# Optimization experiments

Measured on AMD Instinct MI355X. Metric: run time of the kernel, lower is better.

The kernel has to match this reference:

```python
import jax, jax.numpy as jnp
import numpy as np

HEAD_DIM = 64
N_HEADS = 16


def _rope_tables(seq_len, head_dim):
    pos = np.arange(seq_len, dtype=np.float32)
    freq = np.arange(0, head_dim, 2, dtype=np.float32) / head_dim
    inv_freq = 1.0 / (10000.0 ** freq)
    angles = np.outer(pos, inv_freq)                     # [S, D/2]
    angles = np.repeat(angles, 2, axis=-1)               # [S, D] interleaved
    return jnp.asarray(np.cos(angles)), jnp.asarray(np.sin(angles))


def _rotate_half(x):
    x1 = x[..., ::2]
    x2 = x[..., 1::2]
    return jnp.stack((-x2, x1), axis=-1).reshape(x.shape)


def _apply_rope(x, cos, sin):
    # x: [B, H, S, D]; cos/sin: [S, D]
    return x * cos + _rotate_half(x) * sin


def setup_inputs() -> dict:
    key = jax.random.key(0)
    ks = jax.random.split(key, 5)
    d = N_HEADS * HEAD_DIM
    B, S = 4, 2048
    s = 1.0 / np.sqrt(d)
    return {
        "x": jax.random.normal(ks[0], (B, S, d), dtype=jnp.float32),
        "Wq": jax.random.normal(ks[1], (d, d), dtype=jnp.float32) * s,
        "bq": jnp.zeros((d,), jnp.float32),
        "Wk": jax.random.normal(ks[2], (d, d), dtype=jnp.float32) * s,
        "bk": jnp.zeros((d,), jnp.float32),
        "Wv": jax.random.normal(ks[3], (d, d), dtype=jnp.float32) * s,
        "bv": jnp.zeros((d,), jnp.float32),
        "Wo": jax.random.normal(ks[4], (d, d), dtype=jnp.float32) * s,
        "bo": jnp.zeros((d,), jnp.float32),
    }


def reference(x, Wq, bq, Wk, bk, Wv, bv, Wo, bo):
    B, S, d = x.shape
    H, D = N_HEADS, HEAD_DIM
    scale = D ** -0.5

    q = (x @ Wq + bq).reshape(B, S, H, D).transpose(0, 2, 1, 3)  # [B,H,S,D]
    k = (x @ Wk + bk).reshape(B, S, H, D).transpose(0, 2, 1, 3)
    v = (x @ Wv + bv).reshape(B, S, H, D).transpose(0, 2, 1, 3)

    cos, sin = _rope_tables(S, D)
    q = _apply_rope(q, cos, sin)
    k = _apply_rope(k, cos, sin)

    att = jnp.einsum("bhqd,bhkd->bhqk", q, k) * scale            # [B,H,S,S]
    causal = jnp.tril(jnp.ones((S, S), dtype=bool))
    att = jnp.where(causal, att, -jnp.inf)
    att = jax.nn.softmax(att, axis=-1)

    y = jnp.einsum("bhqk,bhkd->bhqd", att, v)                    # [B,H,S,D]
    y = y.transpose(0, 2, 1, 3).reshape(B, S, d)
    return y @ Wo + bo
```

## Files before the change

### kernel.cpp

```cpp
#include <hip/hip_runtime.h>

typedef __bf16 bf16;
typedef __bf16 bf16x2 __attribute__((ext_vector_type(2)));
typedef __bf16 bf16x4 __attribute__((ext_vector_type(4)));
typedef __bf16 bf16x8 __attribute__((ext_vector_type(8)));
typedef float  f32x4  __attribute__((ext_vector_type(4)));

#define MFMA16(a,b,c) __builtin_amdgcn_mfma_f32_16x16x32_bf16(a,b,c,0,0,0)
#define GLL16(g, l) __builtin_amdgcn_global_load_lds( \
    (const __attribute__((address_space(1))) unsigned char*)(g), \
    (__attribute__((address_space(3))) unsigned char*)(l), 16, 0, 0)
#define BARRIER() asm volatile("s_barrier" ::: "memory")
#define DRAIN(n)  asm volatile("s_waitcnt vmcnt(" #n ")" ::: "memory")

constexpr int SEQ   = 2048;
constexpr int NH    = 16;
constexpr int HD    = 64;
constexpr int BATCH = 4;
constexpr int DM    = 1024;
constexpr size_t TEN = (size_t)BATCH * NH * SEQ * HD;

__global__ __launch_bounds__(256) void k_prep(const float* __restrict__ x,
                                              const float* __restrict__ W0,
                                              const float* __restrict__ W1,
                                              const float* __restrict__ W2,
                                              const float* __restrict__ W3,
                                              bf16* __restrict__ Wt_all,
                                              bf16* __restrict__ xb) {
    __shared__ float T[64][65];
    const int z = blockIdx.z;
    const int t = threadIdx.x;
    if (z == 4) {
        const int bi = blockIdx.y * 16 + blockIdx.x;
#pragma unroll
        for (int c = 0; c < 16; c++) {
            const size_t idx = (size_t)c * 524288 + ((size_t)bi * 256 + t) * 8;
            float4 f0 = *(const float4*)(x + idx);
            float4 f1 = *(const float4*)(x + idx + 4);
            bf16x8 o;
            o[0] = (bf16)f0.x; o[1] = (bf16)f0.y; o[2] = (bf16)f0.z; o[3] = (bf16)f0.w;
            o[4] = (bf16)f1.x; o[5] = (bf16)f1.y; o[6] = (bf16)f1.z; o[7] = (bf16)f1.w;
            *(bf16x8*)(xb + idx) = o;
        }
        return;
    }
    const float* W = (z == 0) ? W0 : (z == 1) ? W1 : (z == 2) ? W2 : W3;
    bf16* Wt = Wt_all + (size_t)z * DM * DM;
    const int kb = blockIdx.x, nb = blockIdx.y;
    const int rl = t >> 2, seg = t & 3;
    const float* src = W + (size_t)(kb * 64 + rl) * DM + nb * 64 + seg * 16;
#pragma unroll
    for (int j4 = 0; j4 < 4; j4++) {
        float4 f = *(const float4*)(src + j4 * 4);
        T[rl][seg * 16 + j4 * 4 + 0] = f.x;
        T[rl][seg * 16 + j4 * 4 + 1] = f.y;
        T[rl][seg * 16 + j4 * 4 + 2] = f.z;
        T[rl][seg * 16 + j4 * 4 + 3] = f.w;
    }
    __syncthreads();
    bf16* dst = Wt + (size_t)(nb * 64 + rl) * DM + kb * 64 + seg * 16;
    bf16x8 o0, o1;
#pragma unroll
    for (int j = 0; j < 8; j++) {
        o0[j] = (bf16)T[seg * 16 + j][rl];
        o1[j] = (bf16)T[seg * 16 + 8 + j][rl];
    }
    *(bf16x8*)dst = o0;
    *(bf16x8*)(dst + 8) = o1;
}

template <int MODE>
__global__ __launch_bounds__(512, 1) void k_gemm(const bf16* __restrict__ A,
                                                 const bf16* __restrict__ Wt0,
                                                 const float* __restrict__ b0,
                                                 const float* __restrict__ b1,
                                                 const float* __restrict__ b2,
                                                 bf16* __restrict__ vt,
                                                 void* __restrict__ out) {
    __shared__ __align__(1024) bf16 LA[3][16384];
    __shared__ __align__(1024) bf16 LB[2][8192];
    const int t = threadIdx.x;
    const int w = t >> 6, lane = t & 63, quad = lane >> 4, l16 = lane & 15;
    const int bm = blockIdx.x * 256;
    const int by = blockIdx.y;
    const int z  = (MODE == 0) ? (by >> 3) : 0;
    const int bn = (MODE == 0) ? ((by & 7) * 128) : (by * 128);
    const bf16* Wt = Wt0 + (size_t)z * DM * DM;
    const float* bias = (z == 0) ? b0 : (z == 1) ? b1 : b2;
    const int wm = (w >> 2) * 128, wn = (w & 3) * 32;

    const int srow = lane >> 3;
    const int sseg = (lane & 7) ^ srow;
    const bf16* gA = A  + (size_t)(bm + w * 8 + srow) * DM + sseg * 8;
    const bf16* gB = Wt + (size_t)(bn + w * 8 + srow) * DM + sseg * 8;

#define STGA_P(lp, tt, c) do { \
    const bf16* _g = gA + (size_t)(c) * 128 * DM + (size_t)(tt) * 64; \
    bf16* _l = (lp) + ((c) * 16 + w) * 512; \
    GLL16(_g, _l); GLL16(_g + 64 * DM, _l + 4096); \
} while (0)
#define STGB_P(lp, tt) do { \
    const bf16* _g = gB + (size_t)(tt) * 64; \
    bf16* _l = (lp) + w * 512; \
    GLL16(_g, _l); GLL16(_g + 64 * DM, _l + 4096); \
} while (0)

    const int sA0 = (quad ^ (l16 & 7)) << 3;
    const int sA1 = ((4 + quad) ^ (l16 & 7)) << 3;

    f32x4 zero = {0.f, 0.f, 0.f, 0.f};
    f32x4 acc[8][2];
#pragma unroll
    for (int mt = 0; mt < 8; mt++)
#pragma unroll
        for (int nt = 0; nt < 2; nt++) acc[mt][nt] = zero;
    bf16x8 bfr[2][2];

#define PH(la_, lb_, mb, READB, STAGE_STMT, DRAIN_STMT) do { \
    const bf16* _la = (la_); \
    if (READB) { \
        const bf16* _lb = (lb_); \
        _Pragma("unroll") \
        for (int nt = 0; nt < 2; nt++) { \
            const int r = (wn + nt * 16 + l16) * 64; \
            bfr[nt][0] = *(const bf16x8*)(_lb + r + sA0); \
            bfr[nt][1] = *(const bf16x8*)(_lb + r + sA1); \
        } \
    } \
    bf16x8 af[4][2]; \
    _Pragma("unroll") \
    for (int mi = 0; mi < 4; mi++) { \
        const int r = (wm + ((mb) + mi) * 16 + l16) * 64; \
        af[mi][0] = *(const bf16x8*)(_la + r + sA0); \
        af[mi][1] = *(const bf16x8*)(_la + r + sA1); \
    } \
    STAGE_STMT; \
    DRAIN_STMT; \
    BARRIER(); \
    __builtin_amdgcn_s_setprio(1); \
    _Pragma("unroll") \
    for (int mi = 0; mi < 4; mi++) \
        _Pragma("unroll") \
        for (int nt = 0; nt < 2; nt++) { \
            f32x4 a = acc[(mb) + mi][nt]; \
            a = MFMA16(af[mi][0], bfr[nt][0], a); \
            a = MFMA16(af[mi][1], bfr[nt][1], a); \
            acc[(mb) + mi][nt] = a; \
        } \
    __builtin_amdgcn_s_setprio(0); \
    BARRIER(); \
} while (0)

    STGA_P(&LA[0][0], 0, 0); STGA_P(&LA[0][0], 0, 1); STGB_P(&LB[0][0], 0);
    STGA_P(&LA[1][0], 1, 0); STGA_P(&LA[1][0], 1, 1); STGB_P(&LB[1][0], 1);
    DRAIN(6);
    BARRIER();

    int ae = 0, ao = 1, an = 2;
    for (int i = 0; i < 8; i++) {
        const int tE = (i < 7) ? 2 * i + 2 : 15;
        const int tO = (i < 7) ? 2 * i + 3 : 15;
        bf16* lae = &LA[0][0] + ae * 16384;
        bf16* lao = &LA[0][0] + ao * 16384;
        bf16* lan = &LA[0][0] + an * 16384;
        PH(lae, &LB[0][0], 0, 1, { STGA_P(lan, tE, 0); STGA_P(lan, tE, 1); }, );
        PH(lae, (const bf16*)0, 4, 0, STGB_P(&LB[0][0], tE), DRAIN(6));
        PH(lao, &LB[1][0], 0, 1, { STGA_P(lae, tO, 0); STGA_P(lae, tO, 1); }, );
        PH(lao, (const bf16*)0, 4, 0, STGB_P(&LB[1][0], tO), DRAIN(6));
        const int tmp = ae; ae = an; an = ao; ao = tmp;
    }
#undef PH
#undef STGA_P
#undef STGB_P

    float bv[2], invf[2];
#pragma unroll
    for (int nt = 0; nt < 2; nt++) {
        const int col = bn + wn + nt * 16 + l16;
        bv[nt] = bias[col];
        if (MODE == 0) {
            const int ip = (col & 63) >> 1;
            invf[nt] = __builtin_exp2f(-0.41524101186092029f * (float)ip);
        }
    }
    const int odd = l16 & 1;

    if (MODE == 0 && z == 2) {
#pragma unroll
        for (int mt = 0; mt < 8; mt++) {
            const int row0 = bm + wm + mt * 16 + quad * 4;
            const int b = row0 >> 11, s0 = row0 & (SEQ - 1);
#pragma unroll
            for (int nt = 0; nt < 2; nt++) {
                const int col = bn + wn + nt * 16 + l16;
                const int h = col >> 6, dd = col & 63;
                bf16x4 o;
#pragma unroll
                for (int rg = 0; rg < 4; rg++) o[rg] = (bf16)(acc[mt][nt][rg] + bv[nt]);
                *(bf16x4*)(vt + ((size_t)((b * NH + h) * HD + dd)) * SEQ + s0) = o;
            }
        }
        return;
    }

#pragma unroll
    for (int mt = 0; mt < 8; mt++) {
#pragma unroll
        for (int nt = 0; nt < 2; nt++) {
            const int col = bn + wn + nt * 16 + l16;
#pragma unroll
            for (int rg = 0; rg < 4; rg++) {
                const int row = bm + wm + mt * 16 + quad * 4 + rg;
                float val = acc[mt][nt][rg] + bv[nt];
                if (MODE == 0) {
                    const int b = row >> 11, s = row & (SEQ - 1);
                    const int h = col >> 6, dd = col & 63;
                    const float partner = __shfl_xor(val, 1);
                    float sn, cs;
                    __sincosf((float)s * invf[nt], &sn, &cs);
                    val = odd ? (val * cs + partner * sn)
                              : (val * cs - partner * sn);
                    if (z == 0) val *= 0.125f;
                    ((bf16*)out)[(size_t)z * TEN +
                                 (((size_t)(b * NH + h)) * SEQ + s) * HD + dd] = (bf16)val;
                } else {
                    ((float*)out)[(size_t)row * DM + col] = val;
                }
            }
        }
    }
}

__global__ __launch_bounds__(256, 3) void k_attn(const bf16* __restrict__ q,
                                                 const bf16* __restrict__ k,
                                                 const bf16* __restrict__ vt,
                                                 bf16* __restrict__ y) {
    __shared__ __align__(1024) bf16 KsF[2][4096];
    __shared__ __align__(1024) bf16 VsF[2][4096];
    __shared__ __align__(1024) bf16 PsF[4 * 32 * 64];
    const int t = threadIdx.x;
    const int w = t >> 6, lane = t & 63, quad = lane >> 4, l16 = lane & 15;
    const int bh = blockIdx.x;
    const int qb = 15 - (int)blockIdx.y;
    const int b = bh >> 4, h = bh & 15;

    const int srow = lane >> 3;
    const int gseg = (lane & 7) ^ srow;
    const int c0 = w, c1 = w + 4;

    const bf16* kbase = k  + (size_t)bh * SEQ * HD;
    const bf16* vbase = vt + (size_t)bh * HD * SEQ;
    const float NEG_INF = -__builtin_inff();

    const int koff0 = (c0 * 8 + srow) * HD + gseg * 8;
    const int koff1 = (c1 * 8 + srow) * HD + gseg * 8;
    const int voff0 = (c0 * 8 + srow) * SEQ + gseg * 8;
    const int voff1 = (c1 * 8 + srow) * SEQ + gseg * 8;

#define STGKV(buf, tt) do { \
    GLL16(kbase + (size_t)(tt) * 64 * HD + koff0, &KsF[buf][c0 * 512]); \
    GLL16(kbase + (size_t)(tt) * 64 * HD + koff1, &KsF[buf][c1 * 512]); \
    GLL16(vbase + (size_t)(tt) * 64 + voff0, &VsF[buf][c0 * 512]); \
    GLL16(vbase + (size_t)(tt) * 64 + voff1, &VsF[buf][c1 * 512]); \
} while (0)

    bf16x8 qf[2][2];
#pragma unroll
    for (int mt = 0; mt < 2; mt++) {
        const bf16* qrow = q + ((size_t)bh * SEQ + qb * 128 + w * 32 + mt * 16 + l16) * HD;
        qf[mt][0] = *(const bf16x8*)(qrow + quad * 8);
        qf[mt][1] = *(const bf16x8*)(qrow + 32 + quad * 8);
    }

    const int ktmax = 2 * qb + 1;
    STGKV(0, 0);
    STGKV(1, 1);

    int off_kv[4][2];
#pragma unroll
    for (int nt = 0; nt < 4; nt++) {
        const int r = nt * 16 + l16;
#pragma unroll
        for (int hh = 0; hh < 2; hh++) {
            const int sg = hh * 4 + quad;
            off_kv[nt][hh] = r * 64 + ((sg ^ (r & 7)) << 3);
        }
    }
    const bf16 *pf_p[2][2];
#pragma unroll
    for (int mt = 0; mt < 2; mt++) {
        const int r = mt * 16 + l16;
#pragma unroll
        for (int hh = 0; hh < 2; hh++) {
            const int sg = hh * 4 + quad;
            pf_p[mt][hh] = PsF + w * 2048 + r * 64 + ((sg ^ (r & 7)) << 3);
        }
    }

    f32x4 zero = {0.f, 0.f, 0.f, 0.f};
    f32x4 minus10 = {-10.f, -10.f, -10.f, -10.f};
    f32x4 acc_o[2][4];
    float l_acc[2][4];
#pragma unroll
    for (int mt = 0; mt < 2; mt++)
#pragma unroll
        for (int nt = 0; nt < 4; nt++) acc_o[mt][nt] = zero;
#pragma unroll
    for (int mt = 0; mt < 2; mt++)
#pragma unroll
        for (int rg = 0; rg < 4; rg++) l_acc[mt][rg] = 0.f;

    DRAIN(4);
    BARRIER();

    for (int kt = 0; kt <= ktmax; kt++) {
        const int cur = kt & 1;
        const bf16* kb_ = &KsF[0][0] + cur * 4096;
        const bf16* vb_ = &VsF[0][0] + cur * 4096;

        const int d = qb * 128 + w * 32 - kt * 64;
        if (d > -32) {
            f32x4 accs[2][4];
            __builtin_amdgcn_s_setprio(1);
#pragma unroll
            for (int nt = 0; nt < 4; nt++) {
                const bf16x8 kf0 = *(const bf16x8*)(kb_ + off_kv[nt][0]);
                const bf16x8 kf1 = *(const bf16x8*)(kb_ + off_kv[nt][1]);
#pragma unroll
                for (int mt = 0; mt < 2; mt++) {
                    f32x4 a = minus10;
                    a = MFMA16(qf[mt][0], kf0, a);
                    a = MFMA16(qf[mt][1], kf1, a);
                    accs[mt][nt] = a;
                }
            }
            __builtin_amdgcn_s_setprio(0);
            if (d < 64) {
#pragma unroll
                for (int mt = 0; mt < 2; mt++) {
                    const int qr = d + mt * 16 + quad * 4;
#pragma unroll
                    for (int nt = 0; nt < 4; nt++) {
                        const int kv = nt * 16 + l16;
#pragma unroll
                        for (int rg = 0; rg < 4; rg++)
                            if (kv > qr + rg) accs[mt][nt][rg] = NEG_INF;
                    }
                }
            }
#pragma unroll
            for (int mt = 0; mt < 2; mt++) {
#pragma unroll
                for (int nt = 0; nt < 4; nt++) {
#pragma unroll
                    for (int rg = 0; rg < 4; rg++) {
                        const float p = __expf(accs[mt][nt][rg]);
                        l_acc[mt][rg] += p;
                        const int prow = mt * 16 + quad * 4 + rg;
                        const int psg  = (nt * 2 + (l16 >> 3)) ^ (prow & 7);
                        PsF[w * 2048 + prow * 64 + psg * 8 + (l16 & 7)] = (bf16)p;
                    }
                }
            }
            bf16x8 pf[2][2];
#pragma unroll
            for (int mt = 0; mt < 2; mt++) {
                pf[mt][0] = *(const bf16x8*)pf_p[mt][0];
                pf[mt][1] = *(const bf16x8*)pf_p[mt][1];
            }
            __builtin_amdgcn_s_setprio(1);
#pragma unroll
            for (int nt = 0; nt < 4; nt++) {
                const bf16x8 vf0 = *(const bf16x8*)(vb_ + off_kv[nt][0]);
                const bf16x8 vf1 = *(const bf16x8*)(vb_ + off_kv[nt][1]);
#pragma unroll
                for (int mt = 0; mt < 2; mt++) {
                    acc_o[mt][nt] = MFMA16(pf[mt][0], vf0, acc_o[mt][nt]);
                    acc_o[mt][nt] = MFMA16(pf[mt][1], vf1, acc_o[mt][nt]);
                }
            }
            __builtin_amdgcn_s_setprio(0);
        }
        if (kt < ktmax) {
            BARRIER();
            const int ts = (kt + 2 > ktmax) ? ktmax : (kt + 2);
            STGKV(cur, ts);
            DRAIN(4);
            BARRIER();
        }
    }
#undef STGKV

#pragma unroll
    for (int mt = 0; mt < 2; mt++) {
#pragma unroll
        for (int rg = 0; rg < 4; rg++) {
            float rs = l_acc[mt][rg];
            rs += __shfl_xor(rs, 1);
            rs += __shfl_xor(rs, 2);
            rs += __shfl_xor(rs, 4);
            rs += __shfl_xor(rs, 8);
            const float inv = 1.0f / rs;
            const int s = qb * 128 + w * 32 + mt * 16 + quad * 4 + rg;
#pragma unroll
            for (int nt = 0; nt < 4; nt++) {
                const float val = acc_o[mt][nt][rg] * inv;
                y[((size_t)(b * SEQ + s)) * DM + h * HD + nt * 16 + l16] = (bf16)val;
            }
        }
    }
}

extern "C" void kernel_launch(void* const* d_in, const int* in_sizes, int n_in,
                              void* d_out, int out_size, void* d_ws, size_t ws_size,
                              hipStream_t stream) {
    const float* x  = (const float*)d_in[0];
    const float* Wq = (const float*)d_in[1];
    const float* bq = (const float*)d_in[2];
    const float* Wk = (const float*)d_in[3];
    const float* bk = (const float*)d_in[4];
    const float* Wv = (const float*)d_in[5];
    const float* bv = (const float*)d_in[6];
    const float* Wo = (const float*)d_in[7];
    const float* bo = (const float*)d_in[8];

    char* ws = (char*)d_ws;
    bf16* xb   = (bf16*)(ws);
    bf16* wall = (bf16*)(ws + (16ull << 20));
    bf16* qb   = (bf16*)(ws + (24ull << 20));
    bf16* kb   = (bf16*)(ws + (40ull << 20));
    bf16* vtb  = (bf16*)(ws + (72ull << 20));
    bf16* wot  = wall + 3ull * DM * DM;

    k_prep<<<dim3(16, 16, 5), 256, 0, stream>>>(x, Wq, Wk, Wv, Wo, wall, xb);
    k_gemm<0><<<dim3(32, 24), 512, 0, stream>>>(xb, wall, bq, bk, bv, vtb, qb);
    k_attn<<<dim3(64, 16), 256, 0, stream>>>(qb, kb, vtb, xb);
    k_gemm<1><<<dim3(32, 8), 512, 0, stream>>>(xb, wot, bo, bo, bo, vtb, d_out);
}
```

Measured before the change: 242.0 us.

## Switch GEMM to 32x32x16 MFMA with 4x2 warp tiling and triple-buffered stages

Rewrites the projection GEMM inner loop to use 32x32x16 bf16 MFMA instructions on 64x64 per-wave tiles, replacing the 16x16x32 MFMAs on 128x32 per-wave tiles. B tiles are now triple-buffered alongside A, giving a uniform one-barrier-pair-per-k-tile loop with prefetch two stages ahead. LDS offsets are precomputed and the epilogues are remapped to the 32x32 accumulator layout. The aim is fewer LDS fragment reads per MFMA and a simpler pipeline, at the cost of extra LDS for the third B buffer and a new accumulator-to-row mapping that must be correct for the RoPE and V-transpose stores.

```diff
diff --git a/kernel.cpp b/kernel.cpp
--- a/kernel.cpp
+++ b/kernel.cpp
@@ -5,8 +5,10 @@
 typedef __bf16 bf16x4 __attribute__((ext_vector_type(4)));
 typedef __bf16 bf16x8 __attribute__((ext_vector_type(8)));
 typedef float  f32x4  __attribute__((ext_vector_type(4)));
+typedef float  f32x16 __attribute__((ext_vector_type(16)));
 
 #define MFMA16(a,b,c) __builtin_amdgcn_mfma_f32_16x16x32_bf16(a,b,c,0,0,0)
+#define MFMA32(a,b,c) __builtin_amdgcn_mfma_f32_32x32x16_bf16(a,b,c,0,0,0)
 #define GLL16(g, l) __builtin_amdgcn_global_load_lds( \
     (const __attribute__((address_space(1))) unsigned char*)(g), \
     (__attribute__((address_space(3))) unsigned char*)(l), 16, 0, 0)
@@ -78,16 +80,17 @@
                                                  bf16* __restrict__ vt,
                                                  void* __restrict__ out) {
     __shared__ __align__(1024) bf16 LA[3][16384];
-    __shared__ __align__(1024) bf16 LB[2][8192];
+    __shared__ __align__(1024) bf16 LB[3][8192];
     const int t = threadIdx.x;
-    const int w = t >> 6, lane = t & 63, quad = lane >> 4, l16 = lane & 15;
+    const int w = t >> 6, lane = t & 63;
+    const int l31 = lane & 31, hi = lane >> 5;
     const int bm = blockIdx.x * 256;
     const int by = blockIdx.y;
     const int z  = (MODE == 0) ? (by >> 3) : 0;
     const int bn = (MODE == 0) ? ((by & 7) * 128) : (by * 128);
     const bf16* Wt = Wt0 + (size_t)z * DM * DM;
     const float* bias = (z == 0) ? b0 : (z == 1) ? b1 : b2;
-    const int wm = (w >> 2) * 128, wn = (w & 3) * 32;
+    const int wm = (w >> 1) * 64, wn = (w & 1) * 64;
 
     const int srow = lane >> 3;
     const int sseg = (lane & 7) ^ srow;
@@ -104,117 +107,120 @@
     bf16* _l = (lp) + w * 512; \
     GLL16(_g, _l); GLL16(_g + 64 * DM, _l + 4096); \
 } while (0)
-
-    const int sA0 = (quad ^ (l16 & 7)) << 3;
-    const int sA1 = ((4 + quad) ^ (l16 & 7)) << 3;
-
-    f32x4 zero = {0.f, 0.f, 0.f, 0.f};
-    f32x4 acc[8][2];
-#pragma unroll
-    for (int mt = 0; mt < 8; mt++)
-#pragma unroll
-        for (int nt = 0; nt < 2; nt++) acc[mt][nt] = zero;
-    bf16x8 bfr[2][2];
-
-#define PH(la_, lb_, mb, READB, STAGE_STMT, DRAIN_STMT) do { \
-    const bf16* _la = (la_); \
-    if (READB) { \
-        const bf16* _lb = (lb_); \
-        _Pragma("unroll") \
-        for (int nt = 0; nt < 2; nt++) { \
-            const int r = (wn + nt * 16 + l16) * 64; \
-            bfr[nt][0] = *(const bf16x8*)(_lb + r + sA0); \
-            bfr[nt][1] = *(const bf16x8*)(_lb + r + sA1); \
-        } \
-    } \
-    bf16x8 af[4][2]; \
-    _Pragma("unroll") \
-    for (int mi = 0; mi < 4; mi++) { \
-        const int r = (wm + ((mb) + mi) * 16 + l16) * 64; \
-        af[mi][0] = *(const bf16x8*)(_la + r + sA0); \
-        af[mi][1] = *(const bf16x8*)(_la + r + sA1); \
-    } \
-    STAGE_STMT; \
-    DRAIN_STMT; \
-    BARRIER(); \
-    __builtin_amdgcn_s_setprio(1); \
-    _Pragma("unroll") \
-    for (int mi = 0; mi < 4; mi++) \
-        _Pragma("unroll") \
-        for (int nt = 0; nt < 2; nt++) { \
-            f32x4 a = acc[(mb) + mi][nt]; \
-            a = MFMA16(af[mi][0], bfr[nt][0], a); \
-            a = MFMA16(af[mi][1], bfr[nt][1], a); \
-            acc[(mb) + mi][nt] = a; \
-        } \
-    __builtin_amdgcn_s_setprio(0); \
-    BARRIER(); \
+#define STG_T(la, lb, tt) do { \
+    STGA_P((la), (tt), 0); STGA_P((la), (tt), 1); STGB_P((lb), (tt)); \
 } while (0)
 
-    STGA_P(&LA[0][0], 0, 0); STGA_P(&LA[0][0], 0, 1); STGB_P(&LB[0][0], 0);
-    STGA_P(&LA[1][0], 1, 0); STGA_P(&LA[1][0], 1, 1); STGB_P(&LB[1][0], 1);
+    int offA[2][4], offB[2][4];
+#pragma unroll
+    for (int mt = 0; mt < 2; mt++) {
+        const int r = wm + mt * 32 + l31;
+#pragma unroll
+        for (int ks = 0; ks < 4; ks++)
+            offA[mt][ks] = r * 64 + (((2 * ks + hi) ^ (r & 7)) << 3);
+    }
+#pragma unroll
+    for (int nt = 0; nt < 2; nt++) {
+        const int r = wn + nt * 32 + l31;
+#pragma unroll
+        for (int ks = 0; ks < 4; ks++)
+            offB[nt][ks] = r * 64 + (((2 * ks + hi) ^ (r & 7)) << 3);
+    }
+
+    f32x16 acc[2][2];
+#pragma unroll
+    for (int mt = 0; mt < 2; mt++)
+#pragma unroll
+        for (int nt = 0; nt < 2; nt++)
+#pragma unroll
+            for (int rg = 0; rg < 16; rg++) acc[mt][nt][rg] = 0.f;
+
+    STG_T(&LA[0][0], &LB[0][0], 0);
+    STG_T(&LA[1][0], &LB[1][0], 1);
     DRAIN(6);
     BARRIER();
 
-    int ae = 0, ao = 1, an = 2;
-    for (int i = 0; i < 8; i++) {
-        const int tE = (i < 7) ? 2 * i + 2 : 15;
-        const int tO = (i < 7) ? 2 * i + 3 : 15;
-        bf16* lae = &LA[0][0] + ae * 16384;
-        bf16* lao = &LA[0][0] + ao * 16384;
-        bf16* lan = &LA[0][0] + an * 16384;
-        PH(lae, &LB[0][0], 0, 1, { STGA_P(lan, tE, 0); STGA_P(lan, tE, 1); }, );
-        PH(lae, (const bf16*)0, 4, 0, STGB_P(&LB[0][0], tE), DRAIN(6));
-        PH(lao, &LB[1][0], 0, 1, { STGA_P(lae, tO, 0); STGA_P(lae, tO, 1); }, );
-        PH(lao, (const bf16*)0, 4, 0, STGB_P(&LB[1][0], tO), DRAIN(6));
-        const int tmp = ae; ae = an; an = ao; ao = tmp;
-    }
-#undef PH
+#pragma unroll
+    for (int tk = 0; tk < 16; tk++) {
+        const bf16* la = &LA[tk % 3][0];
+        const bf16* lb = &LB[tk % 3][0];
+        bf16x8 af[2][4], bfr[2][4];
+#pragma unroll
+        for (int mt = 0; mt < 2; mt++)
+#pragma unroll
+            for (int ks = 0; ks < 4; ks++) af[mt][ks] = *(const bf16x8*)(la + offA[mt][ks]);
+#pragma unroll
+        for (int nt = 0; nt < 2; nt++)
+#pragma unroll
+            for (int ks = 0; ks < 4; ks++) bfr[nt][ks] = *(const bf16x8*)(lb + offB[nt][ks]);
+        {
+            const int ts = (tk + 2 > 15) ? 15 : (tk + 2);
+            const int nb = (tk + 2) % 3;
+            STG_T(&LA[nb][0], &LB[nb][0], ts);
+        }
+        DRAIN(6);
+        BARRIER();
+        __builtin_amdgcn_s_setprio(1);
+#pragma unroll
+        for (int ks = 0; ks < 4; ks++)
+#pragma unroll
+            for (int mt = 0; mt < 2; mt++)
+#pragma unroll
+                for (int nt = 0; nt < 2; nt++)
+                    acc[mt][nt] = MFMA32(af[mt][ks], bfr[nt][ks], acc[mt][nt]);
+        __builtin_amdgcn_s_setprio(0);
+        BARRIER();
+    }
+#undef STG_T
 #undef STGA_P
 #undef STGB_P
 
     float bv[2], invf[2];
 #pragma unroll
     for (int nt = 0; nt < 2; nt++) {
-        const int col = bn + wn + nt * 16 + l16;
+        const int col = bn + wn + nt * 32 + l31;
         bv[nt] = bias[col];
         if (MODE == 0) {
             const int ip = (col & 63) >> 1;
             invf[nt] = __builtin_exp2f(-0.41524101186092029f * (float)ip);
         }
     }
-    const int odd = l16 & 1;
+    const int odd = l31 & 1;
 
     if (MODE == 0 && z == 2) {
 #pragma unroll
-        for (int mt = 0; mt < 8; mt++) {
-            const int row0 = bm + wm + mt * 16 + quad * 4;
-            const int b = row0 >> 11, s0 = row0 & (SEQ - 1);
+        for (int mt = 0; mt < 2; mt++) {
 #pragma unroll
             for (int nt = 0; nt < 2; nt++) {
-                const int col = bn + wn + nt * 16 + l16;
+                const int col = bn + wn + nt * 32 + l31;
                 const int h = col >> 6, dd = col & 63;
-                bf16x4 o;
-#pragma unroll
-                for (int rg = 0; rg < 4; rg++) o[rg] = (bf16)(acc[mt][nt][rg] + bv[nt]);
-                *(bf16x4*)(vt + ((size_t)((b * NH + h) * HD + dd)) * SEQ + s0) = o;
+#pragma unroll
+                for (int g = 0; g < 4; g++) {
+                    const int row0 = bm + wm + mt * 32 + 8 * g + 4 * hi;
+                    const int b = row0 >> 11, s0 = row0 & (SEQ - 1);
+                    bf16x4 o;
+#pragma unroll
+                    for (int rg = 0; rg < 4; rg++)
+                        o[rg] = (bf16)(acc[mt][nt][g * 4 + rg] + bv[nt]);
+                    *(bf16x4*)(vt + ((size_t)((b * NH + h) * HD + dd)) * SEQ + s0) = o;
+                }
             }
         }
         return;
     }
 
 #pragma unroll
-    for (int mt = 0; mt < 8; mt++) {
+    for (int mt = 0; mt < 2; mt++) {
 #pragma unroll
         for (int nt = 0; nt < 2; nt++) {
-            const int col = bn + wn + nt * 16 + l16;
-#pragma unroll
-            for (int rg = 0; rg < 4; rg++) {
-                const int row = bm + wm + mt * 16 + quad * 4 + rg;
+            const int col = bn + wn + nt * 32 + l31;
+            const int h = col >> 6, dd = col & 63;
+#pragma unroll
+            for (int rg = 0; rg < 16; rg++) {
+                const int row = bm + wm + mt * 32 + (rg & 3) + 8 * (rg >> 2) + 4 * hi;
                 float val = acc[mt][nt][rg] + bv[nt];
                 if (MODE == 0) {
                     const int b = row >> 11, s = row & (SEQ - 1);
-                    const int h = col >> 6, dd = col & 63;
                     const float partner = __shfl_xor(val, 1);
                     float sn, cs;
                     __sincosf((float)s * invf[nt], &sn, &cs);
```

Measured after the change: 255.9 us. 5.7% more time.
